# Optimization experiments

Hardware: AMD Instinct MI355X
Metric: run time of the kernel (lower is better)

## Reference

```python
import jax, jax.numpy as jnp
import numpy as np

FORGET_BIAS = 1.0  # tf.nn.rnn_cell.LSTMCell default


def _lstm_scan(x_btE, W, b, hidden):
    """x: (B,T,E). W: (E+H, 4H), gate order i, j, f, o (TF LSTMCell)."""
    B = x_btE.shape[0]
    h0 = jnp.zeros((B, hidden), x_btE.dtype)
    c0 = jnp.zeros((B, hidden), x_btE.dtype)

    def step(carry, x_t):
        h, c = carry
        z = jnp.concatenate([x_t, h], axis=-1) @ W + b  # (B, 4H)
        i, j, f, o = jnp.split(z, 4, axis=-1)
        c_new = jax.nn.sigmoid(f + FORGET_BIAS) * c + jax.nn.sigmoid(i) * jnp.tanh(j)
        h_new = jax.nn.sigmoid(o) * jnp.tanh(c_new)
        return (h_new, c_new), h_new

    (_, _), hs = jax.lax.scan(step, (h0, c0), jnp.swapaxes(x_btE, 0, 1))
    return jnp.swapaxes(hs, 0, 1)  # (B, T, H)


def setup_inputs() -> dict:
    key = jax.random.key(0)
    ks = jax.random.split(key, 5)
    B, T, V, E, H, C = 256, 120, 50000, 256, 1024, 5
    tokens = jax.random.randint(ks[0], (B, T, 1), 0, V, dtype=jnp.int32)
    embeddings = jax.random.normal(ks[1], (V, E), jnp.float32) * 0.1
    W_lstm = jax.random.normal(ks[2], (E + H, 4 * H), jnp.float32) * (1.0 / np.sqrt(E + H))
    b_lstm = jnp.zeros((4 * H,), jnp.float32)
    U = jax.random.normal(ks[3], (H, C), jnp.float32) * (1.0 / np.sqrt(H))
    b2 = jnp.zeros((C,), jnp.float32)
    return {"tokens": tokens, "embeddings": embeddings, "W_lstm": W_lstm,
            "b_lstm": b_lstm, "U": U, "b2": b2}


def reference(tokens, embeddings, W_lstm, b_lstm, U, b2):
    B, T, F = tokens.shape  # F == n_features == 1
    E = embeddings.shape[1]
    H = U.shape[0]
    # embedding lookup + reshape to (B, T, F*E)
    x = embeddings[tokens].reshape(B, T, F * E)
    outputs = _lstm_scan(x, W_lstm, b_lstm, H)  # (B, T, H); dropout keep_prob=1 -> identity
    preds = outputs.reshape(-1, H) @ U + b2
    return preds.reshape(B, T, -1)  # (B, max_length, n_classes)
```

## Files before the change

kernel.cpp:

```cpp
#include <hip/hip_runtime.h>

typedef unsigned short u16;
typedef unsigned int u32;
typedef unsigned long long u64;
typedef int   v4i  __attribute__((ext_vector_type(4)));
typedef short v8s  __attribute__((ext_vector_type(8)));
typedef float v2f  __attribute__((ext_vector_type(2)));
typedef float v16f __attribute__((ext_vector_type(16)));

#define B_ 256
#define T_ 120
#define E_ 256
#define H_ 1024
#define K_ 1280
#define LDH 1032
#define LDX 264

#define WS_WF   0
#define WS_X    10485760
#define WS_HS   26214400
#define WS_BAR  89128960

__device__ __forceinline__ u16 f2bf(float f) {
    union { float f; u32 u; } v; v.f = f;
    u32 r = v.u + 0x7fffu + ((v.u >> 16) & 1u);
    return (u16)(r >> 16);
}
__device__ __forceinline__ float bf2f(u16 u) {
    union { u32 u; float f; } v; v.u = ((u32)u) << 16; return v.f;
}
__device__ __forceinline__ float fsig(float x) {
    float t = __builtin_amdgcn_exp2f(-1.44269504f * x);
    return __builtin_amdgcn_rcpf(1.0f + t);
}
__device__ __forceinline__ float ftanh_(float x) {
    float xc = fminf(8.0f, fmaxf(-8.0f, x));
    float t = __builtin_amdgcn_exp2f(2.88539008f * xc);
    return (t - 1.0f) * __builtin_amdgcn_rcpf(t + 1.0f);
}
__device__ __forceinline__ void gl_lds16(const void* g, void* l) {
    __builtin_amdgcn_global_load_lds(
        (const __attribute__((address_space(1))) void*)g,
        (__attribute__((address_space(3))) void*)l, 16, 0, 0);
}

__global__ void prep_w(const float* __restrict__ W, u16* __restrict__ Wf) {
    __shared__ u16 tile[32 * 136];
    int bid = blockIdx.x;
    int cid = bid / 5, fo = bid % 5;
    int kh  = cid & 1, g = (cid >> 1) & 3, nc = cid >> 3;
    int colbase = g * 1024 + nc * 32;
    int tid = threadIdx.x;
    int c = tid & 31, r = tid >> 5;

#pragma unroll
    for (int fl = 0; fl < 8; ++fl) {
        int k0 = (2 * (fo * 8 + fl) + kh) * 16;
#pragma unroll
        for (int rr = 0; rr < 2; ++rr) {
            int row = r + rr * 8;
            float v = W[(size_t)(k0 + row) * 4096 + colbase + c];
            tile[c * 136 + fl * 16 + row] = f2bf(v);
        }
    }
    __syncthreads();

    int lane = tid & 63;
#pragma unroll
    for (int pass = 0; pass < 2; ++pass) {
        int fl = (tid >> 6) + pass * 4;
        v4i o = *(const v4i*)&tile[(lane & 31) * 136 + fl * 16 + ((lane >> 5) << 3)];
        *(v4i*)(Wf + (((size_t)(cid * 40 + fo * 8 + fl)) << 9) + lane * 8) = o;
    }
}

__global__ void prep_x(const int* __restrict__ tokens, const float* __restrict__ emb,
                       u16* __restrict__ X) {
    int v   = blockIdx.x * 256 + threadIdx.x;
    int e8  = v & 31;
    int row = v >> 5;
    int t = row >> 8, b = row & 255;
    int tok = tokens[b * T_ + t];
    const float* src = emb + (size_t)tok * E_ + e8 * 8;
    u16 o[8];
#pragma unroll
    for (int j = 0; j < 8; ++j) o[j] = f2bf(src[j]);
    *(v4i*)(X + (size_t)row * E_ + e8 * 8) = *(v4i*)o;
}

__global__ __launch_bounds__(512, 2) void lstm_main(
    const u16* __restrict__ Wf, const u16* __restrict__ X,
    const float* __restrict__ b_lstm, u16* __restrict__ hs,
    u32* __restrict__ bar) {

    __shared__ u16  hbuf[32 * LDH];
    __shared__ u16  xbuf[32 * LDX];
    __shared__ float gates[2 * 4 * 32 * 34];
    __shared__ float bias[128];

    const int tid   = threadIdx.x;
    const int lane  = tid & 63;
    const int wv    = tid >> 6;
    const int g     = wv >> 1;
    const int khalf = wv & 1;
    const int bid   = blockIdx.x;
    const int mchunk = bid & 7;
    const int nc    = bid >> 3;
    const int m0    = mchunk << 5;

    if (tid < 128) bias[tid] = b_lstm[(tid >> 5) * H_ + (nc << 5) + (tid & 31)];

    v8s Wr[40];
    {
        const int cid = nc * 8 + g * 2 + khalf;
        const v4i* wsrc = (const v4i*)(Wf + (size_t)cid * 40 * 512);
#pragma unroll
        for (int f = 0; f < 40; ++f)
            Wr[f] = __builtin_bit_cast(v8s, wsrc[f * 64 + lane]);
    }
#pragma unroll
    for (int f = 0; f < 40; ++f) asm volatile("" : "+v"(Wr[f]));

    {
        const v4i* xs = (const v4i*)(X + (size_t)m0 * E_);
#pragma unroll
        for (int i = 0; i < 2; ++i) {
            int idx = tid + i * 512;
            int r = idx >> 5, c8 = idx & 31;
            *(v4i*)&xbuf[r * LDX + c8 * 8] = xs[r * 32 + c8];
        }
    }
    __syncthreads();

    const u16* Ax = &xbuf[(lane & 31) * LDX + ((lane >> 5) << 3)];
    const u16* Ah = &hbuf[(lane & 31) * LDH + ((lane >> 5) << 3)];

    v16f acc = {0,0,0,0,0,0,0,0,0,0,0,0,0,0,0,0};
#pragma unroll
    for (int f = 0; f < 8; ++f) {
        v8s a = *(const v8s*)(Ax + (2 * f + khalf) * 16);
        acc = __builtin_amdgcn_mfma_f32_32x32x16_bf16(a, Wr[f], acc, 0, 0, 0);
    }

    float cst[2] = {0.f, 0.f};
    const int cm  = tid >> 4;
    const int cn2 = (tid & 15) << 1;
    u32* hs32 = (u32*)hs;

    for (int t = 0; t < T_; ++t) {
        if (t > 0) {
            if (tid == 0) {
                u32* p = &bar[mchunk * T_ + (t - 1)];
                while (__hip_atomic_load(p, __ATOMIC_RELAXED, __HIP_MEMORY_SCOPE_AGENT) < 32u)
                    __builtin_amdgcn_s_sleep(1);
            }
            __syncthreads();
            {
                const u16* srcb = hs + ((size_t)(t - 1) * B_ + m0) * H_;
                int r0 = wv << 2;
#pragma unroll
                for (int half = 0; half < 2; ++half)
#pragma unroll
                    for (int i = 0; i < 4; ++i) {
                        int r = r0 + i;
                        gl_lds16(srcb + (size_t)r * H_ + half * 512 + lane * 8,
                                 &hbuf[r * LDH + half * 512]);
                    }
            }
            asm volatile("s_waitcnt vmcnt(4)\n\ts_barrier" ::: "memory");
#pragma unroll
            for (int f = 8; f < 24; ++f) {
                v8s a = *(const v8s*)(Ah + ((2 * f + khalf) * 16 - 256));
                acc = __builtin_amdgcn_mfma_f32_32x32x16_bf16(a, Wr[f], acc, 0, 0, 0);
            }
            asm volatile("s_waitcnt vmcnt(0)\n\ts_barrier" ::: "memory");
#pragma unroll
            for (int f = 24; f < 40; ++f) {
                v8s a = *(const v8s*)(Ah + ((2 * f + khalf) * 16 - 256));
                acc = __builtin_amdgcn_mfma_f32_32x32x16_bf16(a, Wr[f], acc, 0, 0, 0);
            }
        }

        {
            float* gb = &gates[((khalf << 2) + g) * 1088];
            int col = lane & 31, rq = (lane >> 5) << 2;
#pragma unroll
            for (int reg = 0; reg < 16; ++reg) {
                int row = (reg & 3) + ((reg >> 2) << 3) + rq;
                gb[row * 34 + col] = acc[reg];
            }
        }
        __syncthreads();

        if (t + 1 < T_) {
            const v4i* xs = (const v4i*)(X + ((size_t)(t + 1) * B_ + m0) * E_);
#pragma unroll
            for (int i = 0; i < 2; ++i) {
                int idx = tid + i * 512;
                int r = idx >> 5, c8 = idx & 31;
                *(v4i*)&xbuf[r * LDX + c8 * 8] = xs[r * 32 + c8];
            }
        }

        u32 hpack = 0;
        {
            v2f zz[4];
#pragma unroll
            for (int gg = 0; gg < 4; ++gg) {
                v2f a = *(const v2f*)&gates[gg * 1088 + cm * 34 + cn2];
                v2f b = *(const v2f*)&gates[(4 + gg) * 1088 + cm * 34 + cn2];
                zz[gg].x = a.x + b.x; zz[gg].y = a.y + b.y;
            }
#pragma unroll
            for (int q = 0; q < 2; ++q) {
                int n = cn2 + q;
                float ip = zz[0][q] + bias[n];
                float jp = zz[1][q] + bias[32 + n];
                float fp = zz[2][q] + bias[64 + n] + 1.0f;
                float op = zz[3][q] + bias[96 + n];
                float cc = fsig(fp) * cst[q] + fsig(ip) * ftanh_(jp);
                cst[q] = cc;
                hpack |= ((u32)f2bf(fsig(op) * ftanh_(cc))) << (16 * q);
            }
        }
        __hip_atomic_store(&hs32[((size_t)t * B_ + m0 + cm) * 512 + (nc << 4) + (tid & 15)],
                           hpack, __ATOMIC_RELAXED, __HIP_MEMORY_SCOPE_AGENT);

        if (t + 1 < T_) {
            asm volatile("s_waitcnt vmcnt(0)" ::: "memory");
            __syncthreads();
            if (tid == 0)
                __hip_atomic_fetch_add(&bar[mchunk * T_ + t], 1u,
                                       __ATOMIC_RELAXED, __HIP_MEMORY_SCOPE_AGENT);
#pragma unroll
            for (int reg = 0; reg < 16; ++reg) acc[reg] = 0.f;
#pragma unroll
            for (int f = 0; f < 8; ++f) {
                v8s a = *(const v8s*)(Ax + (2 * f + khalf) * 16);
                acc = __builtin_amdgcn_mfma_f32_32x32x16_bf16(a, Wr[f], acc, 0, 0, 0);
            }
        }
    }
}

__global__ void proj_kernel(const u16* __restrict__ hs, const float* __restrict__ U,
                            const float* __restrict__ b2, float* __restrict__ out) {
    __shared__ float Ul[H_ * 5];
    int tid = threadIdx.x;
    for (int i = tid; i < H_ * 5; i += 256) Ul[i] = U[i];
    __syncthreads();
    int wv = tid >> 6, lane = tid & 63;
#pragma unroll 1
    for (int i = 0; i < 16; ++i) {
        int row = blockIdx.x * 64 + wv * 16 + i;
        int t = row >> 8, b = row & 255;
        const v4i* hp = (const v4i*)(hs + (size_t)row * H_);
        float p[5] = {0.f, 0.f, 0.f, 0.f, 0.f};
#pragma unroll
        for (int half = 0; half < 2; ++half) {
            v4i hv = hp[lane * 2 + half];
            u16 us[8];
            *(v4i*)us = hv;
#pragma unroll
            for (int j = 0; j < 8; ++j) {
                float hf = bf2f(us[j]);
                int k = lane * 16 + half * 8 + j;
#pragma unroll
                for (int c = 0; c < 5; ++c) p[c] += hf * Ul[k * 5 + c];
            }
        }
#pragma unroll
        for (int c = 0; c < 5; ++c)
            for (int off = 32; off > 0; off >>= 1)
                p[c] += __shfl_down(p[c], off, 64);
        if (lane == 0) {
#pragma unroll
            for (int c = 0; c < 5; ++c)
                out[((size_t)b * T_ + t) * 5 + c] = p[c] + b2[c];
        }
    }
}

extern "C" void kernel_launch(void* const* d_in, const int* in_sizes, int n_in,
                              void* d_out, int out_size, void* d_ws, size_t ws_size,
                              hipStream_t stream) {
    const int*   tokens = (const int*)d_in[0];
    const float* emb    = (const float*)d_in[1];
    const float* W      = (const float*)d_in[2];
    const float* b_l    = (const float*)d_in[3];
    const float* U      = (const float*)d_in[4];
    const float* b2     = (const float*)d_in[5];
    float* out = (float*)d_out;

    char* ws = (char*)d_ws;
    u16* Wf  = (u16*)(ws + WS_WF);
    u16* X   = (u16*)(ws + WS_X);
    u16* hs  = (u16*)(ws + WS_HS);
    u32* bar = (u32*)(ws + WS_BAR);

    hipMemsetAsync(bar, 0, 8 * T_ * sizeof(u32), stream);
    prep_w<<<1280, 256, 0, stream>>>(W, Wf);
    prep_x<<<3840, 256, 0, stream>>>(tokens, emb, X);
    lstm_main<<<256, 512, 0, stream>>>(Wf, X, b_l, hs, bar);
    proj_kernel<<<480, 256, 0, stream>>>(hs, U, b2, out);
}
```

Measured before the change: 610.5 us.

## Use XCD-local L2 barriers when each batch chunk's blocks share one XCD

At startup every block records which XCD it runs on and then runs a trial barrier, so the kernel can tell whether all 32 blocks of an mchunk sit on the same XCD. When they do, the per-timestep barrier polls with sc0 L2 loads and counts with workgroup-scope atomics, and the h stores become plain stores. This avoids device-scope coherence traffic on the critical path of the sequential timesteps. The cost is a startup handshake and reliance on the dispatch mapping and on L2 coherence behaviour. The barrier buffer may also fall back to d_out, which proj later overwrites.

```diff
diff --git a/kernel.cpp b/kernel.cpp
--- a/kernel.cpp
+++ b/kernel.cpp
@@ -21,6 +21,8 @@
 #define WS_HS   26214400
 #define WS_BAR  89128960
 
+#define GETREG_XCC_ID 6164
+
 __device__ __forceinline__ u16 f2bf(float f) {
     union { float f; u32 u; } v; v.f = f;
     u32 r = v.u + 0x7fffu + ((v.u >> 16) & 1u);
@@ -42,6 +44,13 @@
     __builtin_amdgcn_global_load_lds(
         (const __attribute__((address_space(1))) void*)g,
         (__attribute__((address_space(3))) void*)l, 16, 0, 0);
+}
+__device__ __forceinline__ u32 l2_poll(const u32* p) {
+    u64 pa = (u64)p;
+    u32 v;
+    asm volatile("global_load_dword %0, %1, off sc0\n\ts_waitcnt vmcnt(0)"
+                 : "=v"(v) : "v"(pa) : "memory");
+    return v;
 }
 
 __global__ void prep_w(const float* __restrict__ W, u16* __restrict__ Wf) {
@@ -91,12 +100,13 @@
 __global__ __launch_bounds__(512, 2) void lstm_main(
     const u16* __restrict__ Wf, const u16* __restrict__ X,
     const float* __restrict__ b_lstm, u16* __restrict__ hs,
-    u32* __restrict__ bar) {
+    u32* __restrict__ bar, u32* __restrict__ boot) {
 
     __shared__ u16  hbuf[32 * LDH];
     __shared__ u16  xbuf[32 * LDX];
     __shared__ float gates[2 * 4 * 32 * 34];
     __shared__ float bias[128];
+    __shared__ u32 fastflag;
 
     const int tid   = threadIdx.x;
     const int lane  = tid & 63;
@@ -108,6 +118,15 @@
     const int nc    = bid >> 3;
     const int m0    = mchunk << 5;
 
+    if (tid == 0) {
+        u32 xcd = __builtin_amdgcn_s_getreg(GETREG_XCC_ID) & 15u;
+        __hip_atomic_fetch_or(&boot[mchunk], 1u << xcd,
+                              __ATOMIC_RELAXED, __HIP_MEMORY_SCOPE_AGENT);
+        asm volatile("s_waitcnt vmcnt(0)" ::: "memory");
+        __hip_atomic_fetch_add(&boot[16], 1u,
+                               __ATOMIC_RELAXED, __HIP_MEMORY_SCOPE_AGENT);
+    }
+
     if (tid < 128) bias[tid] = b_lstm[(tid >> 5) * H_ + (nc << 5) + (tid & 31)];
 
     v8s Wr[40];
@@ -130,7 +149,38 @@
             *(v4i*)&xbuf[r * LDX + c8 * 8] = xs[r * 32 + c8];
         }
     }
+
+    if (tid == 0) {
+        while (__hip_atomic_load(&boot[16], __ATOMIC_RELAXED,
+                                 __HIP_MEMORY_SCOPE_AGENT) < 256u)
+            __builtin_amdgcn_s_sleep(1);
+        u32 msk = __hip_atomic_load(&boot[mchunk], __ATOMIC_RELAXED,
+                                    __HIP_MEMORY_SCOPE_AGENT);
+        u32 hw_ok = (msk != 0u && (msk & (msk - 1u)) == 0u) ? 1u : 0u;
+
+        u32 trial_ok = 0u;
+        if (hw_ok) {
+            __hip_atomic_fetch_add(&boot[8 + mchunk], 1u,
+                                   __ATOMIC_RELAXED, __HIP_MEMORY_SCOPE_WORKGROUP);
+            for (int it = 0; it < 4000; ++it) {
+                if (l2_poll(&boot[8 + mchunk]) >= 32u) { trial_ok = 1u; break; }
+                __builtin_amdgcn_s_sleep(1);
+            }
+        }
+
+        __hip_atomic_fetch_add(&boot[17], (1u << 16) | (hw_ok & trial_ok),
+                               __ATOMIC_RELAXED, __HIP_MEMORY_SCOPE_AGENT);
+        u32 w;
+        for (;;) {
+            w = __hip_atomic_load(&boot[17], __ATOMIC_RELAXED,
+                                  __HIP_MEMORY_SCOPE_AGENT);
+            if ((w >> 16) >= 256u) break;
+            __builtin_amdgcn_s_sleep(1);
+        }
+        fastflag = ((w & 0xFFFFu) == 256u) ? 1u : 0u;
+    }
     __syncthreads();
+    const bool fast = (fastflag != 0u);
 
     const u16* Ax = &xbuf[(lane & 31) * LDX + ((lane >> 5) << 3)];
     const u16* Ah = &hbuf[(lane & 31) * LDH + ((lane >> 5) << 3)];
@@ -150,9 +200,14 @@
     for (int t = 0; t < T_; ++t) {
         if (t > 0) {
             if (tid == 0) {
-                u32* p = &bar[mchunk * T_ + (t - 1)];
-                while (__hip_atomic_load(p, __ATOMIC_RELAXED, __HIP_MEMORY_SCOPE_AGENT) < 32u)
-                    __builtin_amdgcn_s_sleep(1);
+                u32* p = &bar[mchunk * 128 + (t - 1)];
+                if (fast) {
+                    while (l2_poll(p) < 32u) __builtin_amdgcn_s_sleep(1);
+                } else {
+                    while (__hip_atomic_load(p, __ATOMIC_RELAXED,
+                                             __HIP_MEMORY_SCOPE_AGENT) < 32u)
+                        __builtin_amdgcn_s_sleep(1);
+                }
             }
             __syncthreads();
             {
@@ -223,15 +278,27 @@
                 hpack |= ((u32)f2bf(fsig(op) * ftanh_(cc))) << (16 * q);
             }
         }
-        __hip_atomic_store(&hs32[((size_t)t * B_ + m0 + cm) * 512 + (nc << 4) + (tid & 15)],
-                           hpack, __ATOMIC_RELAXED, __HIP_MEMORY_SCOPE_AGENT);
+        {
+            size_t oidx = ((size_t)t * B_ + m0 + cm) * 512 + (nc << 4) + (tid & 15);
+            if (fast) {
+                hs32[oidx] = hpack;
+            } else {
+                __hip_atomic_store(&hs32[oidx], hpack, __ATOMIC_RELAXED,
+                                   __HIP_MEMORY_SCOPE_AGENT);
+            }
+        }
 
         if (t + 1 < T_) {
             asm volatile("s_waitcnt vmcnt(0)" ::: "memory");
             __syncthreads();
-            if (tid == 0)
-                __hip_atomic_fetch_add(&bar[mchunk * T_ + t], 1u,
-                                       __ATOMIC_RELAXED, __HIP_MEMORY_SCOPE_AGENT);
+            if (tid == 0) {
+                if (fast)
+                    __hip_atomic_fetch_add(&bar[mchunk * 128 + t], 1u,
+                                           __ATOMIC_RELAXED, __HIP_MEMORY_SCOPE_WORKGROUP);
+                else
+                    __hip_atomic_fetch_add(&bar[mchunk * 128 + t], 1u,
+                                           __ATOMIC_RELAXED, __HIP_MEMORY_SCOPE_AGENT);
+            }
 #pragma unroll
             for (int reg = 0; reg < 16; ++reg) acc[reg] = 0.f;
 #pragma unroll
@@ -296,11 +363,15 @@
     u16* Wf  = (u16*)(ws + WS_WF);
     u16* X   = (u16*)(ws + WS_X);
     u16* hs  = (u16*)(ws + WS_HS);
-    u32* bar = (u32*)(ws + WS_BAR);
-
-    hipMemsetAsync(bar, 0, 8 * T_ * sizeof(u32), stream);
+
+    u32* bar;
+    if (ws_size >= (size_t)WS_BAR + 4096 + 96) bar = (u32*)(ws + WS_BAR);
+    else                                       bar = (u32*)d_out;
+    u32* boot = bar + 1024;
+
+    hipMemsetAsync(bar, 0, 4096 + 96, stream);
     prep_w<<<1280, 256, 0, stream>>>(W, Wf);
     prep_x<<<3840, 256, 0, stream>>>(tokens, emb, X);
-    lstm_main<<<256, 512, 0, stream>>>(Wf, X, b_l, hs, bar);
+    lstm_main<<<256, 512, 0, stream>>>(Wf, X, b_l, hs, bar, boot);
     proj_kernel<<<480, 256, 0, stream>>>(hs, U, b2, out);
 }
```

Result: slower. 968.2 us (+58.6%).

## Fuse prep kernels and fold output projection into the recurrent LSTM loop

Applied to the files above, without the earlier changes.

Merges weight conversion, embedding gather and barrier zeroing into one prep launch, replacing two kernels and a memset. The separate projection kernel is removed. Each LSTM block now computes its own row of the 5-class projection from the h tile already staged in LDS during the next timestep. The final timestep is handled after an extra grid-level wait. This cuts launch count and avoids re-reading all hidden states from global memory. In exchange it adds 20KB of LDS for U plus reductions and a store on the serial recurrent critical path.

```diff
diff --git a/kernel.cpp b/kernel.cpp
--- a/kernel.cpp
+++ b/kernel.cpp
@@ -44,59 +44,69 @@
         (__attribute__((address_space(3))) void*)l, 16, 0, 0);
 }
 
-__global__ void prep_w(const float* __restrict__ W, u16* __restrict__ Wf) {
+__global__ void prep_fused(const float* __restrict__ W, u16* __restrict__ Wf,
+                           const int* __restrict__ tokens, const float* __restrict__ emb,
+                           u16* __restrict__ X, u32* __restrict__ bar) {
     __shared__ u16 tile[32 * 136];
-    int bid = blockIdx.x;
-    int cid = bid / 5, fo = bid % 5;
-    int kh  = cid & 1, g = (cid >> 1) & 3, nc = cid >> 3;
-    int colbase = g * 1024 + nc * 32;
+    int bx  = blockIdx.x;
     int tid = threadIdx.x;
-    int c = tid & 31, r = tid >> 5;
-
-#pragma unroll
-    for (int fl = 0; fl < 8; ++fl) {
-        int k0 = (2 * (fo * 8 + fl) + kh) * 16;
-#pragma unroll
-        for (int rr = 0; rr < 2; ++rr) {
-            int row = r + rr * 8;
-            float v = W[(size_t)(k0 + row) * 4096 + colbase + c];
-            tile[c * 136 + fl * 16 + row] = f2bf(v);
-        }
-    }
-    __syncthreads();
-
-    int lane = tid & 63;
-#pragma unroll
-    for (int pass = 0; pass < 2; ++pass) {
-        int fl = (tid >> 6) + pass * 4;
-        v4i o = *(const v4i*)&tile[(lane & 31) * 136 + fl * 16 + ((lane >> 5) << 3)];
-        *(v4i*)(Wf + (((size_t)(cid * 40 + fo * 8 + fl)) << 9) + lane * 8) = o;
-    }
-}
-
-__global__ void prep_x(const int* __restrict__ tokens, const float* __restrict__ emb,
-                       u16* __restrict__ X) {
-    int v   = blockIdx.x * 256 + threadIdx.x;
-    int e8  = v & 31;
-    int row = v >> 5;
-    int t = row >> 8, b = row & 255;
-    int tok = tokens[b * T_ + t];
-    const float* src = emb + (size_t)tok * E_ + e8 * 8;
-    u16 o[8];
-#pragma unroll
-    for (int j = 0; j < 8; ++j) o[j] = f2bf(src[j]);
-    *(v4i*)(X + (size_t)row * E_ + e8 * 8) = *(v4i*)o;
+
+    if (bx < 1280) {
+        if (bx == 0) {
+            v4i z = {0, 0, 0, 0};
+            *(v4i*)(bar + tid * 4) = z;
+        }
+        int cid = bx / 5, fo = bx % 5;
+        int kh  = cid & 1, g = (cid >> 1) & 3, nc = cid >> 3;
+        int colbase = g * 1024 + nc * 32;
+        int c = tid & 31, r = tid >> 5;
+
+#pragma unroll
+        for (int fl = 0; fl < 8; ++fl) {
+            int k0 = (2 * (fo * 8 + fl) + kh) * 16;
+#pragma unroll
+            for (int rr = 0; rr < 2; ++rr) {
+                int row = r + rr * 8;
+                float v = W[(size_t)(k0 + row) * 4096 + colbase + c];
+                tile[c * 136 + fl * 16 + row] = f2bf(v);
+            }
+        }
+        __syncthreads();
+
+        int lane = tid & 63;
+#pragma unroll
+        for (int pass = 0; pass < 2; ++pass) {
+            int fl = (tid >> 6) + pass * 4;
+            v4i o = *(const v4i*)&tile[(lane & 31) * 136 + fl * 16 + ((lane >> 5) << 3)];
+            *(v4i*)(Wf + (((size_t)(cid * 40 + fo * 8 + fl)) << 9) + lane * 8) = o;
+        }
+    } else {
+        int v   = (bx - 1280) * 256 + tid;
+        int e8  = v & 31;
+        int row = v >> 5;
+        int t = row >> 8, b = row & 255;
+        int tok = tokens[b * T_ + t];
+        const float* src = emb + (size_t)tok * E_ + e8 * 8;
+        u16 o[8];
+#pragma unroll
+        for (int j = 0; j < 8; ++j) o[j] = f2bf(src[j]);
+        *(v4i*)(X + (size_t)row * E_ + e8 * 8) = *(v4i*)o;
+    }
 }
 
 __global__ __launch_bounds__(512, 2) void lstm_main(
     const u16* __restrict__ Wf, const u16* __restrict__ X,
     const float* __restrict__ b_lstm, u16* __restrict__ hs,
-    u32* __restrict__ bar) {
+    u32* __restrict__ bar, const float* __restrict__ U,
+    const float* __restrict__ b2, float* __restrict__ out) {
 
     __shared__ u16  hbuf[32 * LDH];
     __shared__ u16  xbuf[32 * LDX];
     __shared__ float gates[2 * 4 * 32 * 34];
     __shared__ float bias[128];
+    __shared__ float Ul[H_ * 5];
+    __shared__ float b2l[5];
+    __shared__ float pscr[40];
 
     const int tid   = threadIdx.x;
     const int lane  = tid & 63;
@@ -109,6 +119,8 @@
     const int m0    = mchunk << 5;
 
     if (tid < 128) bias[tid] = b_lstm[(tid >> 5) * H_ + (nc << 5) + (tid & 31)];
+    for (int i = tid; i < H_ * 5; i += 512) Ul[i] = U[i];
+    if (tid < 5) b2l[tid] = b2[tid];
 
     v8s Wr[40];
     {
@@ -179,6 +191,26 @@
                 v8s a = *(const v8s*)(Ah + ((2 * f + khalf) * 16 - 256));
                 acc = __builtin_amdgcn_mfma_f32_32x32x16_bf16(a, Wr[f], acc, 0, 0, 0);
             }
+
+            {
+                u32 hv = *(const u32*)&hbuf[nc * LDH + (tid << 1)];
+                float h0 = bf2f((u16)(hv & 0xffffu));
+                float h1 = bf2f((u16)(hv >> 16));
+                int k = tid << 1;
+                float pp[5];
+#pragma unroll
+                for (int c = 0; c < 5; ++c)
+                    pp[c] = h0 * Ul[k * 5 + c] + h1 * Ul[(k + 1) * 5 + c];
+#pragma unroll
+                for (int c = 0; c < 5; ++c)
+#pragma unroll
+                    for (int off = 32; off > 0; off >>= 1)
+                        pp[c] += __shfl_down(pp[c], off, 64);
+                if (lane == 0) {
+#pragma unroll
+                    for (int c = 0; c < 5; ++c) pscr[wv * 5 + c] = pp[c];
+                }
+            }
         }
 
         {
@@ -191,6 +223,13 @@
             }
         }
         __syncthreads();
+
+        if (t > 0 && tid < 5) {
+            float s = 0.f;
+#pragma unroll
+            for (int w = 0; w < 8; ++w) s += pscr[w * 5 + tid];
+            out[((size_t)(m0 + nc) * T_ + (t - 1)) * 5 + tid] = s + b2l[tid];
+        }
 
         if (t + 1 < T_) {
             const v4i* xs = (const v4i*)(X + ((size_t)(t + 1) * B_ + m0) * E_);
@@ -241,43 +280,55 @@
             }
         }
     }
-}
-
-__global__ void proj_kernel(const u16* __restrict__ hs, const float* __restrict__ U,
-                            const float* __restrict__ b2, float* __restrict__ out) {
-    __shared__ float Ul[H_ * 5];
-    int tid = threadIdx.x;
-    for (int i = tid; i < H_ * 5; i += 256) Ul[i] = U[i];
+
+    asm volatile("s_waitcnt vmcnt(0)" ::: "memory");
     __syncthreads();
-    int wv = tid >> 6, lane = tid & 63;
-#pragma unroll 1
-    for (int i = 0; i < 16; ++i) {
-        int row = blockIdx.x * 64 + wv * 16 + i;
-        int t = row >> 8, b = row & 255;
-        const v4i* hp = (const v4i*)(hs + (size_t)row * H_);
-        float p[5] = {0.f, 0.f, 0.f, 0.f, 0.f};
-#pragma unroll
-        for (int half = 0; half < 2; ++half) {
-            v4i hv = hp[lane * 2 + half];
-            u16 us[8];
-            *(v4i*)us = hv;
-#pragma unroll
-            for (int j = 0; j < 8; ++j) {
-                float hf = bf2f(us[j]);
-                int k = lane * 16 + half * 8 + j;
-#pragma unroll
-                for (int c = 0; c < 5; ++c) p[c] += hf * Ul[k * 5 + c];
-            }
-        }
+    if (tid == 0) {
+        __hip_atomic_fetch_add(&bar[mchunk * T_ + (T_ - 1)], 1u,
+                               __ATOMIC_RELAXED, __HIP_MEMORY_SCOPE_AGENT);
+        u32* p = &bar[mchunk * T_ + (T_ - 1)];
+        while (__hip_atomic_load(p, __ATOMIC_RELAXED, __HIP_MEMORY_SCOPE_AGENT) < 32u)
+            __builtin_amdgcn_s_sleep(1);
+    }
+    __syncthreads();
+    {
+        const u16* srcb = hs + ((size_t)(T_ - 1) * B_ + m0) * H_;
+        int r0 = wv << 2;
+#pragma unroll
+        for (int half = 0; half < 2; ++half)
+#pragma unroll
+            for (int i = 0; i < 4; ++i) {
+                int r = r0 + i;
+                gl_lds16(srcb + (size_t)r * H_ + half * 512 + lane * 8,
+                         &hbuf[r * LDH + half * 512]);
+            }
+    }
+    asm volatile("s_waitcnt vmcnt(0)\n\ts_barrier" ::: "memory");
+    {
+        u32 hv = *(const u32*)&hbuf[nc * LDH + (tid << 1)];
+        float h0 = bf2f((u16)(hv & 0xffffu));
+        float h1 = bf2f((u16)(hv >> 16));
+        int k = tid << 1;
+        float pp[5];
 #pragma unroll
         for (int c = 0; c < 5; ++c)
+            pp[c] = h0 * Ul[k * 5 + c] + h1 * Ul[(k + 1) * 5 + c];
+#pragma unroll
+        for (int c = 0; c < 5; ++c)
+#pragma unroll
             for (int off = 32; off > 0; off >>= 1)
-                p[c] += __shfl_down(p[c], off, 64);
+                pp[c] += __shfl_down(pp[c], off, 64);
         if (lane == 0) {
 #pragma unroll
-            for (int c = 0; c < 5; ++c)
-                out[((size_t)b * T_ + t) * 5 + c] = p[c] + b2[c];
-        }
+            for (int c = 0; c < 5; ++c) pscr[wv * 5 + c] = pp[c];
+        }
+    }
+    __syncthreads();
+    if (tid < 5) {
+        float s = 0.f;
+#pragma unroll
+        for (int w = 0; w < 8; ++w) s += pscr[w * 5 + tid];
+        out[((size_t)(m0 + nc) * T_ + (T_ - 1)) * 5 + tid] = s + b2l[tid];
     }
 }
 
@@ -298,9 +349,6 @@
     u16* hs  = (u16*)(ws + WS_HS);
     u32* bar = (u32*)(ws + WS_BAR);
 
-    hipMemsetAsync(bar, 0, 8 * T_ * sizeof(u32), stream);
-    prep_w<<<1280, 256, 0, stream>>>(W, Wf);
-    prep_x<<<3840, 256, 0, stream>>>(tokens, emb, X);
-    lstm_main<<<256, 512, 0, stream>>>(Wf, X, b_l, hs, bar);
-    proj_kernel<<<480, 256, 0, stream>>>(hs, U, b2, out);
-}
+    prep_fused<<<5120, 256, 0, stream>>>(W, Wf, tokens, emb, X, bar);
+    lstm_main<<<256, 512, 0, stream>>>(Wf, X, b_l, hs, bar, U, b2, out);
+}
```

Result: slower. 682.5 us (+11.8%).

## Replace atomic-add step barrier with per-block flag stores; fuse prep kernels

Applied to the files above, without the earlier changes.

Cross-block step synchronization now has each producer block store its completed step index into its own padded flag slot. A whole wavefront polls the 32 flags of its row chunk and uses a wave vote to decide when to proceed, replacing one shared atomic counter per step. The memset and the two prep kernels are merged into one launch, which zeroes the flags itself. This removes atomic contention and launch overhead, at the cost of more polling traffic per waiting block.

```diff
diff --git a/kernel.cpp b/kernel.cpp
--- a/kernel.cpp
+++ b/kernel.cpp
@@ -44,48 +44,54 @@
         (__attribute__((address_space(3))) void*)l, 16, 0, 0);
 }
 
-__global__ void prep_w(const float* __restrict__ W, u16* __restrict__ Wf) {
+__global__ void prep_fused(const float* __restrict__ W, u16* __restrict__ Wf,
+                           const int* __restrict__ tokens, const float* __restrict__ emb,
+                           u16* __restrict__ X, u32* __restrict__ bar) {
     __shared__ u16 tile[32 * 136];
-    int bid = blockIdx.x;
-    int cid = bid / 5, fo = bid % 5;
-    int kh  = cid & 1, g = (cid >> 1) & 3, nc = cid >> 3;
-    int colbase = g * 1024 + nc * 32;
+    int bx  = blockIdx.x;
     int tid = threadIdx.x;
-    int c = tid & 31, r = tid >> 5;
-
-#pragma unroll
-    for (int fl = 0; fl < 8; ++fl) {
-        int k0 = (2 * (fo * 8 + fl) + kh) * 16;
-#pragma unroll
-        for (int rr = 0; rr < 2; ++rr) {
-            int row = r + rr * 8;
-            float v = W[(size_t)(k0 + row) * 4096 + colbase + c];
-            tile[c * 136 + fl * 16 + row] = f2bf(v);
-        }
-    }
-    __syncthreads();
-
-    int lane = tid & 63;
-#pragma unroll
-    for (int pass = 0; pass < 2; ++pass) {
-        int fl = (tid >> 6) + pass * 4;
-        v4i o = *(const v4i*)&tile[(lane & 31) * 136 + fl * 16 + ((lane >> 5) << 3)];
-        *(v4i*)(Wf + (((size_t)(cid * 40 + fo * 8 + fl)) << 9) + lane * 8) = o;
-    }
-}
-
-__global__ void prep_x(const int* __restrict__ tokens, const float* __restrict__ emb,
-                       u16* __restrict__ X) {
-    int v   = blockIdx.x * 256 + threadIdx.x;
-    int e8  = v & 31;
-    int row = v >> 5;
-    int t = row >> 8, b = row & 255;
-    int tok = tokens[b * T_ + t];
-    const float* src = emb + (size_t)tok * E_ + e8 * 8;
-    u16 o[8];
-#pragma unroll
-    for (int j = 0; j < 8; ++j) o[j] = f2bf(src[j]);
-    *(v4i*)(X + (size_t)row * E_ + e8 * 8) = *(v4i*)o;
+
+    if (bx < 1280) {
+        if (bx == 0) {
+            v4i z = {0, 0, 0, 0};
+            *(v4i*)(bar + tid * 4) = z;
+        }
+        int cid = bx / 5, fo = bx % 5;
+        int kh  = cid & 1, g = (cid >> 1) & 3, nc = cid >> 3;
+        int colbase = g * 1024 + nc * 32;
+        int c = tid & 31, r = tid >> 5;
+
+#pragma unroll
+        for (int fl = 0; fl < 8; ++fl) {
+            int k0 = (2 * (fo * 8 + fl) + kh) * 16;
+#pragma unroll
+            for (int rr = 0; rr < 2; ++rr) {
+                int row = r + rr * 8;
+                float v = W[(size_t)(k0 + row) * 4096 + colbase + c];
+                tile[c * 136 + fl * 16 + row] = f2bf(v);
+            }
+        }
+        __syncthreads();
+
+        int lane = tid & 63;
+#pragma unroll
+        for (int pass = 0; pass < 2; ++pass) {
+            int fl = (tid >> 6) + pass * 4;
+            v4i o = *(const v4i*)&tile[(lane & 31) * 136 + fl * 16 + ((lane >> 5) << 3)];
+            *(v4i*)(Wf + (((size_t)(cid * 40 + fo * 8 + fl)) << 9) + lane * 8) = o;
+        }
+    } else {
+        int v   = (bx - 1280) * 256 + tid;
+        int e8  = v & 31;
+        int row = v >> 5;
+        int t = row >> 8, b = row & 255;
+        int tok = tokens[b * T_ + t];
+        const float* src = emb + (size_t)tok * E_ + e8 * 8;
+        u16 o[8];
+#pragma unroll
+        for (int j = 0; j < 8; ++j) o[j] = f2bf(src[j]);
+        *(v4i*)(X + (size_t)row * E_ + e8 * 8) = *(v4i*)o;
+    }
 }
 
 __global__ __launch_bounds__(512, 2) void lstm_main(
@@ -149,10 +155,14 @@
 
     for (int t = 0; t < T_; ++t) {
         if (t > 0) {
-            if (tid == 0) {
-                u32* p = &bar[mchunk * T_ + (t - 1)];
-                while (__hip_atomic_load(p, __ATOMIC_RELAXED, __HIP_MEMORY_SCOPE_AGENT) < 32u)
+            if (wv == 0) {
+                u32* p = &bar[(mchunk * 32 + (lane & 31)) * 4];
+                for (;;) {
+                    u32 v = __hip_atomic_load(p, __ATOMIC_RELAXED,
+                                              __HIP_MEMORY_SCOPE_AGENT);
+                    if (__all(v >= (u32)t)) break;
                     __builtin_amdgcn_s_sleep(1);
+                }
             }
             __syncthreads();
             {
@@ -230,8 +240,8 @@
             asm volatile("s_waitcnt vmcnt(0)" ::: "memory");
             __syncthreads();
             if (tid == 0)
-                __hip_atomic_fetch_add(&bar[mchunk * T_ + t], 1u,
-                                       __ATOMIC_RELAXED, __HIP_MEMORY_SCOPE_AGENT);
+                __hip_atomic_store(&bar[(mchunk * 32 + nc) * 4], (u32)(t + 1),
+                                   __ATOMIC_RELAXED, __HIP_MEMORY_SCOPE_AGENT);
 #pragma unroll
             for (int reg = 0; reg < 16; ++reg) acc[reg] = 0.f;
 #pragma unroll
@@ -298,9 +308,7 @@
     u16* hs  = (u16*)(ws + WS_HS);
     u32* bar = (u32*)(ws + WS_BAR);
 
-    hipMemsetAsync(bar, 0, 8 * T_ * sizeof(u32), stream);
-    prep_w<<<1280, 256, 0, stream>>>(W, Wf);
-    prep_x<<<3840, 256, 0, stream>>>(tokens, emb, X);
+    prep_fused<<<5120, 256, 0, stream>>>(W, Wf, tokens, emb, X, bar);
     lstm_main<<<256, 512, 0, stream>>>(Wf, X, b_l, hs, bar);
     proj_kernel<<<480, 256, 0, stream>>>(hs, U, b2, out);
 }
```

New measurement: 581.0 us, median of 2. 4.8% less time.
